# Kernel optimization log

Measured on AMD Instinct MI355X. Metric: run time of the kernel, lower is better.

The kernel has to match this reference:

```python
import jax, jax.numpy as jnp
import numpy as np
import math

D_MODEL = 1024
N_HEAD = 16


def setup_inputs() -> dict:
    key = jax.random.key(0)
    ks = jax.random.split(key, 12)
    B, T, D = 4, 2048, D_MODEL
    s = 1.0 / math.sqrt(D)
    return {
        "q": jax.random.normal(ks[0], (B, T, D), jnp.float32),
        "k": jax.random.normal(ks[1], (B, T, D), jnp.float32),
        "v": jax.random.normal(ks[2], (B, T, D), jnp.float32),
        "w_q": jax.random.normal(ks[3], (D, D), jnp.float32) * s,
        "b_q": jnp.zeros((D,), jnp.float32),
        "w_k": jax.random.normal(ks[4], (D, D), jnp.float32) * s,
        "b_k": jnp.zeros((D,), jnp.float32),
        "w_v": jax.random.normal(ks[5], (D, D), jnp.float32) * s,
        "b_v": jnp.zeros((D,), jnp.float32),
        "w_o": jax.random.normal(ks[6], (D, D), jnp.float32) * s,
        "b_o": jnp.zeros((D,), jnp.float32),
    }


def reference(q, k, v, w_q, b_q, w_k, b_k, w_v, b_v, w_o, b_o):
    B, T, D = q.shape
    H = N_HEAD
    n_d = D // H
    # QKV projections (torch Linear: x @ W.T + b; weights here stored as (D,D) applied as x@W + b)
    qh = (q @ w_q + b_q).reshape(B, T, H, n_d).transpose(0, 2, 1, 3)  # [B,H,T,nd]
    kh = (k @ w_k + b_k).reshape(B, T, H, n_d).transpose(0, 2, 1, 3)
    vh = (v @ w_v + b_v).reshape(B, T, H, n_d).transpose(0, 2, 1, 3)
    score = jnp.einsum("bhqd,bhkd->bhqk", qh, kh) / jnp.sqrt(jnp.float32(n_d))
    attn = jax.nn.softmax(score, axis=-1)
    out = jnp.einsum("bhqk,bhkd->bhqd", attn, vh)  # [B,H,T,nd]
    out = out.transpose(0, 2, 1, 3).reshape(B, T, D)
    return out @ w_o + b_o
```

## Files before the change

### kernel.cpp

```cpp
#include <hip/hip_runtime.h>
#include <hip/hip_bf16.h>
#include <stdint.h>

#define D_MODEL 1024
#define NHEAD   16
#define BATCH   4
#define SEQ     2048
#define M_TOK   (BATCH*SEQ)

#define QSCALE  0.18033688011112042f

typedef __attribute__((ext_vector_type(8))) short bf16x8;
typedef __attribute__((ext_vector_type(4))) float f32x4;

static __device__ __forceinline__ unsigned short f2b(float x) {
  union { float f; unsigned int u; } a; a.f = x;
  unsigned int u = a.u;
  u += 0x7FFFu + ((u >> 16) & 1u);
  return (unsigned short)(u >> 16);
}

static __device__ __forceinline__ unsigned int cvt_pk_bf16(float lo, float hi) {
  unsigned int r;
  asm("v_cvt_pk_bf16_f32 %0, %1, %2" : "=v"(r) : "v"(lo), "v"(hi));
  return r;
}

typedef const __attribute__((address_space(1))) unsigned int g_u32;
typedef __attribute__((address_space(3))) unsigned int l_u32;
static __device__ __forceinline__ void glds16(const void* g, void* l) {
  __builtin_amdgcn_global_load_lds((g_u32*)g, (l_u32*)l, 16, 0, 0);
}

__global__ void k_wtrans(const float* __restrict__ w0, const float* __restrict__ w1,
                         const float* __restrict__ w2, const float* __restrict__ w3,
                         unsigned short* __restrict__ wt) {
  __shared__ float tile[32][33];
  int z = blockIdx.z;
  const float* w = (z == 0) ? w0 : (z == 1) ? w1 : (z == 2) ? w2 : w3;
  unsigned short* out = wt + (size_t)z * D_MODEL * D_MODEL;
  int n0 = blockIdx.x * 32, k0 = blockIdx.y * 32;
  int tx = threadIdx.x;
  int ty = threadIdx.y;
  #pragma unroll
  for (int j = 0; j < 4; ++j)
    tile[ty + 8*j][tx] = w[(long)(k0 + ty + 8*j)*D_MODEL + n0 + tx];
  __syncthreads();
  #pragma unroll
  for (int j = 0; j < 4; ++j)
    out[(long)(n0 + ty + 8*j)*D_MODEL + k0 + tx] = f2b(tile[tx][ty + 8*j]);
}

template<int A_F32, int OUT_BF16>
static __device__ __forceinline__ void gemm_body(
    const void* __restrict__ Aptr,
    const unsigned short* __restrict__ Bt,
    const float* __restrict__ bias,
    void* __restrict__ Cout,
    int Ndim, int Kdim, float scale,
    void* AsRaw, unsigned short* Bs,
    long m0, long n0)
{
  const int tid  = threadIdx.x;
  const int lane = tid & 63;
  const int w    = tid >> 6;
  const int wr   = w >> 1, wc = w & 1;
  const int l15  = lane & 15, lg = lane >> 4;

  f32x4 acc[4][4];
  #pragma unroll
  for (int i = 0; i < 4; ++i)
    #pragma unroll
    for (int j = 0; j < 4; ++j)
      #pragma unroll
      for (int c = 0; c < 4; ++c) acc[i][j][c] = 0.f;

  const int r8 = lane >> 3, c8s = (lane & 7) ^ (r8 & 7);
  const int r4 = lane >> 2, c4s = (lane & 3) ^ (r4 & 3);

  for (int kt = 0; kt < Kdim; kt += 32) {
    if (A_F32) {
      const float* Af = (const float*)Aptr;
      #pragma unroll
      for (int j = 0; j < 4; ++j)
        glds16(Af + (m0 + w*32 + j*8 + r8) * Kdim + kt + c8s*4,
               (float*)AsRaw + (w*32 + j*8) * 32);
    } else {
      const unsigned short* Ab = (const unsigned short*)Aptr;
      #pragma unroll
      for (int j = 0; j < 2; ++j)
        glds16(Ab + (m0 + w*32 + j*16 + r4) * Kdim + kt + c4s*8,
               (unsigned short*)AsRaw + (w*32 + j*16) * 32);
    }
    #pragma unroll
    for (int j = 0; j < 2; ++j)
      glds16(Bt + (n0 + w*32 + j*16 + r4) * Kdim + kt + c4s*8,
             Bs + (w*32 + j*16) * 32);
    __syncthreads();

    bf16x8 af[4], bfr[4];
    #pragma unroll
    for (int m = 0; m < 4; ++m) {
      if (A_F32) {
        const float* base = (const float*)AsRaw + (wr*64 + m*16 + l15) * 32;
        f32x4 lo = *(const f32x4*)(base + (((2*lg    ) ^ (l15 & 7)) * 4));
        f32x4 hi = *(const f32x4*)(base + (((2*lg + 1) ^ (l15 & 7)) * 4));
        union { bf16x8 v; unsigned int u[4]; } tmpu;
        tmpu.u[0] = cvt_pk_bf16(lo[0], lo[1]);
        tmpu.u[1] = cvt_pk_bf16(lo[2], lo[3]);
        tmpu.u[2] = cvt_pk_bf16(hi[0], hi[1]);
        tmpu.u[3] = cvt_pk_bf16(hi[2], hi[3]);
        af[m] = tmpu.v;
      } else {
        af[m] = *(const bf16x8*)((const unsigned short*)AsRaw +
                 (wr*64 + m*16 + l15) * 32 + ((lg ^ (l15 & 3)) * 8));
      }
    }
    #pragma unroll
    for (int n = 0; n < 4; ++n)
      bfr[n] = *(const bf16x8*)&Bs[(wc*64 + n*16 + l15) * 32 + ((lg ^ (l15 & 3)) * 8)];
    #pragma unroll
    for (int m = 0; m < 4; ++m)
      #pragma unroll
      for (int n = 0; n < 4; ++n)
        acc[m][n] = __builtin_amdgcn_mfma_f32_16x16x32_bf16(af[m], bfr[n], acc[m][n], 0, 0, 0);
    __syncthreads();
  }

  #pragma unroll
  for (int m = 0; m < 4; ++m) {
    #pragma unroll
    for (int r = 0; r < 4; ++r) {
      long row = m0 + wr*64 + m*16 + lg*4 + r;
      #pragma unroll
      for (int n = 0; n < 4; ++n) {
        long col = n0 + wc*64 + n*16 + l15;
        float v = (acc[m][n][r] + bias[col]) * scale;
        if (OUT_BF16) ((unsigned short*)Cout)[row * Ndim + col] = f2b(v);
        else          ((float*)Cout)[row * Ndim + col] = v;
      }
    }
  }
}

__global__ __launch_bounds__(256) void k_gemm_qkv(
    const float* __restrict__ q, const float* __restrict__ k, const float* __restrict__ v,
    const unsigned short* __restrict__ wt,
    const float* __restrict__ b_q, const float* __restrict__ b_k, const float* __restrict__ b_v,
    unsigned short* __restrict__ Qp, unsigned short* __restrict__ Kp, unsigned short* __restrict__ Vp)
{
  __shared__ float          Asf[128*32];
  __shared__ unsigned short Bs [128*32];
  int z = blockIdx.z;
  const float* A           = (z == 0) ? q : (z == 1) ? k : v;
  const unsigned short* Bt = wt + (size_t)z * D_MODEL * D_MODEL;
  const float* bias        = (z == 0) ? b_q : (z == 1) ? b_k : b_v;
  unsigned short* Cout     = (z == 0) ? Qp : (z == 1) ? Kp : Vp;
  float scale              = (z == 0) ? QSCALE : 1.f;
  gemm_body<1, 1>(A, Bt, bias, Cout, D_MODEL, D_MODEL, scale, Asf, Bs,
                  (long)blockIdx.y * 128, (long)blockIdx.x * 128);
}

__global__ __launch_bounds__(256) void k_gemm_out(
    const unsigned short* __restrict__ A, const unsigned short* __restrict__ Bt,
    const float* __restrict__ bias, float* __restrict__ Cout)
{
  __shared__ unsigned short As16[128*32];
  __shared__ unsigned short Bs  [128*32];
  gemm_body<0, 0>(A, Bt, bias, Cout, D_MODEL, D_MODEL, 1.f, As16, Bs,
                  (long)blockIdx.y * 128, (long)blockIdx.x * 128);
}

__global__ void k_vtrans(const unsigned short* __restrict__ Vp, unsigned short* __restrict__ Vt) {
  __shared__ unsigned short tile[64][72];
  int bh = blockIdx.y;
  int b = bh >> 4, h = bh & 15;
  int t0 = blockIdx.x * 64;
  int tid = threadIdx.x;
  #pragma unroll
  for (int p = 0; p < 2; ++p) {
    int idx = p*256 + tid;
    int tr = idx >> 3, c8 = (idx & 7) * 8;
    *(int4*)&tile[tr][c8] =
        *(const int4*)&Vp[((long)b*SEQ + t0 + tr)*D_MODEL + h*64 + c8];
  }
  __syncthreads();
  #pragma unroll
  for (int p = 0; p < 2; ++p) {
    int idx = p*256 + tid;
    int d = idx >> 3, c8 = (idx & 7) * 8;
    unsigned short tmp[8];
    #pragma unroll
    for (int j = 0; j < 8; ++j) {
      int pos = c8 + j;
      int src = (pos & 32) + (((pos >> 2) & 1) << 4) + (((pos >> 3) & 3) << 2) + (pos & 3);
      tmp[j] = tile[src][d];
    }
    *(int4*)&Vt[((long)bh*64 + d)*SEQ + t0 + c8] = *(int4*)tmp;
  }
}

__global__ __launch_bounds__(256) void k_attn(
    const unsigned short* __restrict__ Qp,
    const unsigned short* __restrict__ Kp,
    const unsigned short* __restrict__ Vt,
    unsigned short* __restrict__ Ao)
{
  __shared__ unsigned short KV[2][2][64*64];
  const int tid = threadIdx.x;
  const int lane = tid & 63;
  const int w = tid >> 6;
  const int bh = blockIdx.y;
  const int b = bh >> 4, h = bh & 15;
  const int q0 = blockIdx.x * 128;
  const int l15 = lane & 15, lg = lane >> 4;
  const int swz = l15 & 7;

  bf16x8 qf[2][2];
  #pragma unroll
  for (int qb = 0; qb < 2; ++qb) {
    const long qrow = (long)b*SEQ + q0 + w*32 + qb*16 + l15;
    #pragma unroll
    for (int kb = 0; kb < 2; ++kb)
      qf[qb][kb] = *(const bf16x8*)&Qp[qrow*D_MODEL + h*64 + kb*32 + lg*8];
  }

  f32x4 acc[2][4];
  float mrun[2], lrun[2];
  #pragma unroll
  for (int qb = 0; qb < 2; ++qb) {
    #pragma unroll
    for (int nb = 0; nb < 4; ++nb)
      #pragma unroll
      for (int c = 0; c < 4; ++c) acc[qb][nb][c] = 0.f;
    mrun[qb] = -1e30f; lrun[qb] = 0.f;
  }

  const int sr = lane >> 3;
  const int sc = (lane & 7) ^ (sr & 7);
  const unsigned short* Kg = Kp + ((long)b*SEQ + w*16 + sr) * D_MODEL + h*64 + sc*8;
  const unsigned short* Vg = Vt + ((long)bh*64 + w*16 + sr) * SEQ + sc*8;

  const int NT = SEQ / 64;

#define STAGE(t, buf) do {                                              \
    unsigned short* Kb_ = &KV[(buf)][0][0] + w*16*64;                   \
    unsigned short* Vb_ = &KV[(buf)][1][0] + w*16*64;                   \
    glds16(Kg + (long)(t)*64*D_MODEL,                   Kb_);           \
    glds16(Kg + (long)(t)*64*D_MODEL + 8L*D_MODEL,      Kb_ + 8*64);    \
    glds16(Vg + (t)*64,                                 Vb_);           \
    glds16(Vg + (t)*64 + 8*SEQ,                         Vb_ + 8*64);    \
  } while (0)

  STAGE(0, 0);

  for (int t = 0; t < NT; ++t) {
    __syncthreads();
    if (t + 1 < NT) STAGE(t + 1, (t + 1) & 1);
    const unsigned short* Kb = &KV[t & 1][0][0];
    const unsigned short* Vb = &KV[t & 1][1][0];

    f32x4 s[2][4];
    #pragma unroll
    for (int qb = 0; qb < 2; ++qb)
      #pragma unroll
      for (int nb = 0; nb < 4; ++nb)
        #pragma unroll
        for (int c = 0; c < 4; ++c) s[qb][nb][c] = 0.f;
    #pragma unroll
    for (int nb = 0; nb < 4; ++nb) {
      #pragma unroll
      for (int kb = 0; kb < 2; ++kb) {
        bf16x8 kf = *(const bf16x8*)&Kb[(nb*16 + l15)*64 + (((kb*4 + lg) ^ swz) * 8)];
        s[0][nb] = __builtin_amdgcn_mfma_f32_16x16x32_bf16(kf, qf[0][kb], s[0][nb], 0, 0, 0);
        s[1][nb] = __builtin_amdgcn_mfma_f32_16x16x32_bf16(kf, qf[1][kb], s[1][nb], 0, 0, 0);
      }
    }

    bf16x8 pa[2][2];
    #pragma unroll
    for (int qb = 0; qb < 2; ++qb) {
      float pmx = fmaxf(
          fmaxf(fmaxf(fmaxf(s[qb][0][0], s[qb][0][1]), fmaxf(s[qb][0][2], s[qb][0][3])),
                fmaxf(fmaxf(s[qb][1][0], s[qb][1][1]), fmaxf(s[qb][1][2], s[qb][1][3]))),
          fmaxf(fmaxf(fmaxf(s[qb][2][0], s[qb][2][1]), fmaxf(s[qb][2][2], s[qb][2][3])),
                fmaxf(fmaxf(s[qb][3][0], s[qb][3][1]), fmaxf(s[qb][3][2], s[qb][3][3]))));
      pmx = fmaxf(pmx, __shfl_xor(pmx, 16));
      pmx = fmaxf(pmx, __shfl_xor(pmx, 32));
      float mold = mrun[qb];
      float mnew = fmaxf(mold, pmx);
      if (__any(mnew > mold)) {
        float alpha = __builtin_amdgcn_exp2f(mold - mnew);
        mrun[qb] = mnew;
        float alr[4];
        #pragma unroll
        for (int r = 0; r < 4; ++r) alr[r] = __shfl(alpha, lg*4 + r);
        #pragma unroll
        for (int nb = 0; nb < 4; ++nb)
          #pragma unroll
          for (int r = 0; r < 4; ++r) acc[qb][nb][r] *= alr[r];
        lrun[qb] *= alpha;
      }
      const float m = mrun[qb];
      float p[4][4];
      float rs = 0.f;
      #pragma unroll
      for (int nb = 0; nb < 4; ++nb) {
        #pragma unroll
        for (int r = 0; r < 4; ++r) {
          p[nb][r] = __builtin_amdgcn_exp2f(s[qb][nb][r] - m);
          rs += p[nb][r];
        }
      }
      union { bf16x8 v; unsigned int u[4]; } pk0, pk1;
      pk0.u[0] = cvt_pk_bf16(p[0][0], p[0][1]);
      pk0.u[1] = cvt_pk_bf16(p[0][2], p[0][3]);
      pk0.u[2] = cvt_pk_bf16(p[1][0], p[1][1]);
      pk0.u[3] = cvt_pk_bf16(p[1][2], p[1][3]);
      pk1.u[0] = cvt_pk_bf16(p[2][0], p[2][1]);
      pk1.u[1] = cvt_pk_bf16(p[2][2], p[2][3]);
      pk1.u[2] = cvt_pk_bf16(p[3][0], p[3][1]);
      pk1.u[3] = cvt_pk_bf16(p[3][2], p[3][3]);
      pa[qb][0] = pk0.v;
      pa[qb][1] = pk1.v;
      rs += __shfl_xor(rs, 16);
      rs += __shfl_xor(rs, 32);
      lrun[qb] += rs;
    }

    #pragma unroll
    for (int nb = 0; nb < 4; ++nb) {
      #pragma unroll
      for (int kb = 0; kb < 2; ++kb) {
        bf16x8 vf = *(const bf16x8*)&Vb[(nb*16 + l15)*64 + (((kb*4 + lg) ^ swz) * 8)];
        acc[0][nb] = __builtin_amdgcn_mfma_f32_16x16x32_bf16(pa[0][kb], vf, acc[0][nb], 0, 0, 0);
        acc[1][nb] = __builtin_amdgcn_mfma_f32_16x16x32_bf16(pa[1][kb], vf, acc[1][nb], 0, 0, 0);
      }
    }
  }
#undef STAGE

  #pragma unroll
  for (int qb = 0; qb < 2; ++qb) {
    float invl = 1.f / lrun[qb];
    float invr[4];
    #pragma unroll
    for (int r = 0; r < 4; ++r) invr[r] = __shfl(invl, lg*4 + r);
    #pragma unroll
    for (int r = 0; r < 4; ++r) {
      long row = (long)b*SEQ + q0 + w*32 + qb*16 + lg*4 + r;
      #pragma unroll
      for (int nb = 0; nb < 4; ++nb)
        Ao[row*D_MODEL + h*64 + nb*16 + l15] = f2b(acc[qb][nb][r] * invr[r]);
    }
  }
}

extern "C" void kernel_launch(void* const* d_in, const int* in_sizes, int n_in,
                              void* d_out, int out_size, void* d_ws, size_t ws_size,
                              hipStream_t stream) {
  const float* q   = (const float*)d_in[0];
  const float* k   = (const float*)d_in[1];
  const float* v   = (const float*)d_in[2];
  const float* w_q = (const float*)d_in[3];
  const float* b_q = (const float*)d_in[4];
  const float* w_k = (const float*)d_in[5];
  const float* b_k = (const float*)d_in[6];
  const float* w_v = (const float*)d_in[7];
  const float* b_v = (const float*)d_in[8];
  const float* w_o = (const float*)d_in[9];
  const float* b_o = (const float*)d_in[10];

  char* ws = (char*)d_ws;
  const size_t SZ  = (size_t)M_TOK * D_MODEL * 2;
  const size_t WSZ = (size_t)D_MODEL * D_MODEL * 2;
  unsigned short* wt  = (unsigned short*)(ws);
  unsigned short* wt3 = (unsigned short*)(ws + 3*WSZ);
  unsigned short* Qp  = (unsigned short*)(ws + 4*WSZ);
  unsigned short* Kp  = (unsigned short*)(ws + 4*WSZ + SZ);
  unsigned short* Vp  = (unsigned short*)(ws + 4*WSZ + 2*SZ);
  unsigned short* Vt  = (unsigned short*)(ws + 4*WSZ + 3*SZ);
  unsigned short* Ao  = (unsigned short*)(ws + 4*WSZ + 4*SZ);

  k_wtrans<<<dim3(32, 32, 4), dim3(32, 8), 0, stream>>>(w_q, w_k, w_v, w_o, wt);

  dim3 g3(D_MODEL/128, M_TOK/128, 3);
  k_gemm_qkv<<<g3, 256, 0, stream>>>(q, k, v, wt, b_q, b_k, b_v, Qp, Kp, Vp);

  k_vtrans<<<dim3(SEQ/64, BATCH*NHEAD), 256, 0, stream>>>(Vp, Vt);
  k_attn  <<<dim3(SEQ/128, BATCH*NHEAD), 256, 0, stream>>>(Qp, Kp, Vt, Ao);

  dim3 gg(D_MODEL/128, M_TOK/128);
  k_gemm_out<<<gg, 256, 0, stream>>>(Ao, wt3, b_o, (float*)d_out);
}
```

Before: 405.2 us.

## Double-buffer GEMM LDS tiles and remap blocks to XCDs for L2 locality

The GEMM main loop now uses two LDS buffers, issuing the next K-tile's global-to-LDS loads before computing on the current tile, with one barrier per iteration instead of two. This is meant to overlap memory latency with MFMA work, at the cost of doubled LDS use per block, which can lower occupancy. It also remaps block indices for the GEMM and attention kernels so that consecutive tiles sharing A rows or the same head land on the same XCD. That remap is meant to improve L2 reuse across the chiplets.

```diff
diff --git a/kernel.cpp b/kernel.cpp
--- a/kernel.cpp
+++ b/kernel.cpp
@@ -58,7 +58,7 @@
     const float* __restrict__ bias,
     void* __restrict__ Cout,
     int Ndim, int Kdim, float scale,
-    void* AsRaw, unsigned short* Bs,
+    void* As0, void* As1, unsigned short* Bs0, unsigned short* Bs1,
     long m0, long n0)
 {
   const int tid  = threadIdx.x;
@@ -78,31 +78,42 @@
   const int r8 = lane >> 3, c8s = (lane & 7) ^ (r8 & 7);
   const int r4 = lane >> 2, c4s = (lane & 3) ^ (r4 & 3);
 
-  for (int kt = 0; kt < Kdim; kt += 32) {
-    if (A_F32) {
-      const float* Af = (const float*)Aptr;
-      #pragma unroll
-      for (int j = 0; j < 4; ++j)
-        glds16(Af + (m0 + w*32 + j*8 + r8) * Kdim + kt + c8s*4,
-               (float*)AsRaw + (w*32 + j*8) * 32);
-    } else {
-      const unsigned short* Ab = (const unsigned short*)Aptr;
-      #pragma unroll
-      for (int j = 0; j < 2; ++j)
-        glds16(Ab + (m0 + w*32 + j*16 + r4) * Kdim + kt + c4s*8,
-               (unsigned short*)AsRaw + (w*32 + j*16) * 32);
-    }
-    #pragma unroll
-    for (int j = 0; j < 2; ++j)
-      glds16(Bt + (n0 + w*32 + j*16 + r4) * Kdim + kt + c4s*8,
-             Bs + (w*32 + j*16) * 32);
+#define STAGEK(kt_, buf_) do {                                               \
+    void* As_ = (buf_) ? As1 : As0;                                          \
+    unsigned short* Bs_ = (buf_) ? Bs1 : Bs0;                                \
+    if (A_F32) {                                                             \
+      const float* Af = (const float*)Aptr;                                  \
+      _Pragma("unroll")                                                      \
+      for (int j = 0; j < 4; ++j)                                            \
+        glds16(Af + (m0 + w*32 + j*8 + r8) * Kdim + (kt_) + c8s*4,           \
+               (float*)As_ + (w*32 + j*8) * 32);                             \
+    } else {                                                                 \
+      const unsigned short* Ab = (const unsigned short*)Aptr;                \
+      _Pragma("unroll")                                                      \
+      for (int j = 0; j < 2; ++j)                                            \
+        glds16(Ab + (m0 + w*32 + j*16 + r4) * Kdim + (kt_) + c4s*8,          \
+               (unsigned short*)As_ + (w*32 + j*16) * 32);                   \
+    }                                                                        \
+    _Pragma("unroll")                                                        \
+    for (int j = 0; j < 2; ++j)                                              \
+      glds16(Bt + (n0 + w*32 + j*16 + r4) * Kdim + (kt_) + c4s*8,            \
+             Bs_ + (w*32 + j*16) * 32);                                      \
+  } while (0)
+
+  STAGEK(0, 0);
+
+  #pragma unroll 2
+  for (int kt = 0, bu = 0; kt < Kdim; kt += 32, bu ^= 1) {
     __syncthreads();
+    if (kt + 32 < Kdim) STAGEK(kt + 32, bu ^ 1);
+    const void* As_ = bu ? As1 : As0;
+    const unsigned short* Bs_ = bu ? Bs1 : Bs0;
 
     bf16x8 af[4], bfr[4];
     #pragma unroll
     for (int m = 0; m < 4; ++m) {
       if (A_F32) {
-        const float* base = (const float*)AsRaw + (wr*64 + m*16 + l15) * 32;
+        const float* base = (const float*)As_ + (wr*64 + m*16 + l15) * 32;
         f32x4 lo = *(const f32x4*)(base + (((2*lg    ) ^ (l15 & 7)) * 4));
         f32x4 hi = *(const f32x4*)(base + (((2*lg + 1) ^ (l15 & 7)) * 4));
         union { bf16x8 v; unsigned int u[4]; } tmpu;
@@ -112,20 +123,20 @@
         tmpu.u[3] = cvt_pk_bf16(hi[2], hi[3]);
         af[m] = tmpu.v;
       } else {
-        af[m] = *(const bf16x8*)((const unsigned short*)AsRaw +
+        af[m] = *(const bf16x8*)((const unsigned short*)As_ +
                  (wr*64 + m*16 + l15) * 32 + ((lg ^ (l15 & 3)) * 8));
       }
     }
     #pragma unroll
     for (int n = 0; n < 4; ++n)
-      bfr[n] = *(const bf16x8*)&Bs[(wc*64 + n*16 + l15) * 32 + ((lg ^ (l15 & 3)) * 8)];
+      bfr[n] = *(const bf16x8*)&Bs_[(wc*64 + n*16 + l15) * 32 + ((lg ^ (l15 & 3)) * 8)];
     #pragma unroll
     for (int m = 0; m < 4; ++m)
       #pragma unroll
       for (int n = 0; n < 4; ++n)
         acc[m][n] = __builtin_amdgcn_mfma_f32_16x16x32_bf16(af[m], bfr[n], acc[m][n], 0, 0, 0);
-    __syncthreads();
-  }
+  }
+#undef STAGEK
 
   #pragma unroll
   for (int m = 0; m < 4; ++m) {
@@ -141,6 +152,13 @@
       }
     }
   }
+}
+
+static __device__ __forceinline__ void xcd_remap_8x64(int& m, int& n) {
+  int lb = blockIdx.x + (blockIdx.y << 3);
+  int xcd = lb & 7, i = lb >> 3;
+  m = (xcd << 3) | (i >> 3);
+  n = i & 7;
 }
 
 __global__ __launch_bounds__(256) void k_gemm_qkv(
@@ -149,26 +167,28 @@
     const float* __restrict__ b_q, const float* __restrict__ b_k, const float* __restrict__ b_v,
     unsigned short* __restrict__ Qp, unsigned short* __restrict__ Kp, unsigned short* __restrict__ Vp)
 {
-  __shared__ float          Asf[128*32];
-  __shared__ unsigned short Bs [128*32];
+  __shared__ float          Asf[2][128*32];
+  __shared__ unsigned short Bs [2][128*32];
   int z = blockIdx.z;
   const float* A           = (z == 0) ? q : (z == 1) ? k : v;
   const unsigned short* Bt = wt + (size_t)z * D_MODEL * D_MODEL;
   const float* bias        = (z == 0) ? b_q : (z == 1) ? b_k : b_v;
   unsigned short* Cout     = (z == 0) ? Qp : (z == 1) ? Kp : Vp;
   float scale              = (z == 0) ? QSCALE : 1.f;
-  gemm_body<1, 1>(A, Bt, bias, Cout, D_MODEL, D_MODEL, scale, Asf, Bs,
-                  (long)blockIdx.y * 128, (long)blockIdx.x * 128);
+  int m, n; xcd_remap_8x64(m, n);
+  gemm_body<1, 1>(A, Bt, bias, Cout, D_MODEL, D_MODEL, scale,
+                  Asf[0], Asf[1], Bs[0], Bs[1], (long)m * 128, (long)n * 128);
 }
 
 __global__ __launch_bounds__(256) void k_gemm_out(
     const unsigned short* __restrict__ A, const unsigned short* __restrict__ Bt,
     const float* __restrict__ bias, float* __restrict__ Cout)
 {
-  __shared__ unsigned short As16[128*32];
-  __shared__ unsigned short Bs  [128*32];
-  gemm_body<0, 0>(A, Bt, bias, Cout, D_MODEL, D_MODEL, 1.f, As16, Bs,
-                  (long)blockIdx.y * 128, (long)blockIdx.x * 128);
+  __shared__ unsigned short As16[2][128*32];
+  __shared__ unsigned short Bs  [2][128*32];
+  int m, n; xcd_remap_8x64(m, n);
+  gemm_body<0, 0>(A, Bt, bias, Cout, D_MODEL, D_MODEL, 1.f,
+                  As16[0], As16[1], Bs[0], Bs[1], (long)m * 128, (long)n * 128);
 }
 
 __global__ void k_vtrans(const unsigned short* __restrict__ Vp, unsigned short* __restrict__ Vt) {
@@ -210,9 +230,12 @@
   const int tid = threadIdx.x;
   const int lane = tid & 63;
   const int w = tid >> 6;
-  const int bh = blockIdx.y;
+  int lb = blockIdx.x + (blockIdx.y << 4);
+  int xcd = lb & 7, li = lb >> 3;
+  const int bh = (xcd << 3) | (li >> 4);
+  const int qblk = li & 15;
   const int b = bh >> 4, h = bh & 15;
-  const int q0 = blockIdx.x * 128;
+  const int q0 = qblk * 128;
   const int l15 = lane & 15, lg = lane >> 4;
   const int swz = l15 & 7;
 
```

New measurement: 440.6 us. 8.7% more time.
